# Kernel optimization log

Hardware: AMD Instinct MI355X
Metric: run time of the kernel (lower is better)

Reference implementation:

```python
import jax, jax.numpy as jnp
import numpy as np

D, K, HID, NBLK, N = 128, 256, 256, 2, 4096

def setup_inputs() -> dict:
    key = jax.random.key(0)
    ks = jax.random.split(key, 12)
    inp = {
        'x': jax.random.normal(ks[0], (N, D), jnp.float32),
        'x_hat': jax.random.normal(ks[1], (N, D), jnp.float32),
        'base_codebook': jax.random.normal(ks[2], (K, D), jnp.float32) * 0.1,
        # concat_proj: Linear(2D -> D), torch weight layout (out, in)
        'Wp': jax.random.normal(ks[3], (D, 2 * D), jnp.float32) / np.sqrt(2 * D),
        'bp': jnp.zeros((D,), jnp.float32),
        # residual blocks stacked over NBLK: Linear(D->HID), ReLU, Linear(HID->D)
        'W1': jax.random.normal(ks[4], (NBLK, HID, D), jnp.float32) / np.sqrt(D),
        'b1': jnp.zeros((NBLK, HID), jnp.float32),
        'W2': jax.random.normal(ks[5], (NBLK, D, HID), jnp.float32) / np.sqrt(HID),
        'b2': jnp.zeros((NBLK, D), jnp.float32),
    }
    return inp

def _forward(x, x_hat, base_codebook, Wp, bp, W1, b1, W2, b2):
    # concat_proj([x_hat, cbar]) decomposed: avoids materializing (N,K,2D)
    x_part = x_hat @ Wp[:, :D].T                      # (N, D)
    c_part = base_codebook @ Wp[:, D:].T + bp          # (K, D)
    C = x_part[:, None, :] + c_part[None, :, :]        # (N, K, D)
    for i in range(NBLK):
        h = jax.nn.relu(jnp.einsum('nkd,hd->nkh', C, W1[i]) + b1[i])
        C = C + jnp.einsum('nkh,dh->nkd', h, W2[i]) + b2[i]
    r = x - x_hat                                      # (N, D)
    dists = jnp.sum((r[:, None, :] - C) ** 2, axis=-1) # (N, K)
    codes = jnp.argmin(dists, axis=-1)                 # (N,)
    c_sel = jnp.take_along_axis(C, codes[:, None, None], axis=1)[:, 0, :]
    x_hat_new = x_hat + c_sel
    return codes, x_hat_new, r, c_sel

def reference(x, x_hat, base_codebook, Wp, bp, W1, b1, W2, b2):
    return _forward(x, x_hat, base_codebook, Wp, bp, W1, b1, W2, b2)
```

## Files before the change

### kernel.cpp

```cpp
#include <hip/hip_runtime.h>


#define QD    128
#define QK    256
#define QHID  256
#define QNBLK 2
#define QN    4096

typedef _Float16 f16;
typedef _Float16 f16x8  __attribute__((ext_vector_type(8)));
typedef float    f32x16 __attribute__((ext_vector_type(16)));
typedef unsigned u32x2  __attribute__((ext_vector_type(2)));

#define WS_CPART 0
#define WS_W1H   131072
#define WS_W1L   262144
#define WS_W2H   393216
#define WS_W2L   524288

#define L_WBUF  0
#define L_B1    98304
#define L_B2    100352
#define L_REDD  101376
#define L_REDI  102400
#define L_XP    103424
#define L_XH    103936
#define L_RS    104448
#define L_CSEL  104960
#define L_TOTAL 105472

static __device__ __forceinline__ f32x16 MF32(f16x8 a, f16x8 b, f32x16 c) {
    return __builtin_amdgcn_mfma_f32_32x32x16_f16(a, b, c, 0, 0, 0);
}
static __device__ __forceinline__ unsigned pkrtz(float a, float b) {
    return __builtin_bit_cast(unsigned, __builtin_amdgcn_cvt_pkrtz(a, b));
}
static __device__ __forceinline__ float f32lo(unsigned p) {
    return (float)__builtin_bit_cast(f16, (unsigned short)(p & 0xffffu));
}
static __device__ __forceinline__ float f32hi(unsigned p) {
    return (float)__builtin_bit_cast(f16, (unsigned short)(p >> 16));
}
static __device__ __forceinline__ u32x2 plswap(unsigned a, unsigned b) {
    return __builtin_amdgcn_permlane32_swap(a, b, false, false);
}
static __device__ __forceinline__ void gload_lds16(const void* g, void* l) {
    __builtin_amdgcn_global_load_lds(
        (const __attribute__((address_space(1))) unsigned*)g,
        (__attribute__((address_space(3))) unsigned*)l, 16, 0, 0);
}

template<int RB>
static __device__ __forceinline__ void split_frags(f32x16 a, f16x8& fh, f16x8& fl) {
    unsigned P0 = pkrtz(a[RB + 0], a[RB + 1]);
    unsigned P1 = pkrtz(a[RB + 2], a[RB + 3]);
    unsigned Q0 = pkrtz(a[RB + 4], a[RB + 5]);
    unsigned Q1 = pkrtz(a[RB + 6], a[RB + 7]);
    unsigned L0 = pkrtz(a[RB + 0] - f32lo(P0), a[RB + 1] - f32hi(P0));
    unsigned L1 = pkrtz(a[RB + 2] - f32lo(P1), a[RB + 3] - f32hi(P1));
    unsigned L2 = pkrtz(a[RB + 4] - f32lo(Q0), a[RB + 5] - f32hi(Q0));
    unsigned L3 = pkrtz(a[RB + 6] - f32lo(Q1), a[RB + 7] - f32hi(Q1));
    u32x2 s0 = plswap(P0, Q0);
    u32x2 s1 = plswap(P1, Q1);
    u32x2 t0 = plswap(L0, L2);
    u32x2 t1 = plswap(L1, L3);
    uint4 hw = make_uint4(s0.x, s1.x, s0.y, s1.y);
    uint4 lw = make_uint4(t0.x, t1.x, t0.y, t1.y);
    fh = __builtin_bit_cast(f16x8, hw);
    fl = __builtin_bit_cast(f16x8, lw);
}

__global__ __launch_bounds__(128) void qinco_prep(
    const float* __restrict__ cb, const float* __restrict__ Wp,
    const float* __restrict__ bp, const float* __restrict__ W1,
    const float* __restrict__ W2, char* __restrict__ ws) {
    const int blk = blockIdx.x;
    const int t = threadIdx.x;
    __shared__ float row[QD];

    if (blk < 256) {
        float* cpart = (float*)(ws + WS_CPART);
        row[t] = cb[blk * QD + t];
        __syncthreads();
        float acc = bp[t];
        const float* wr = Wp + (size_t)t * (2 * QD) + QD;
        #pragma unroll 8
        for (int e = 0; e < QD; ++e) acc = fmaf(row[e], wr[e], acc);
        cpart[blk * QD + t] = acc;
    } else if (blk < 384) {
        if (t < 64) {
            const int cid = blk - 256;
            const int b = cid >> 6, hc = (cid >> 3) & 7, kc = cid & 7;
            const int m = t & 31, g = t >> 5;
            f16* w1h = (f16*)(ws + WS_W1H);
            f16* w1l = (f16*)(ws + WS_W1L);
            #pragma unroll
            for (int j = 0; j < 8; ++j) {
                float wv = W1[((size_t)b * QHID + hc * 32 + m) * QD + kc * 16 + g * 8 + j];
                f16 hi = (f16)wv;
                size_t idx = ((size_t)cid * 64 + t) * 8 + j;
                w1h[idx] = hi;
                w1l[idx] = (f16)(wv - (float)hi);
            }
        }
    } else {
        if (t < 64) {
            const int e = blk - 384;
            const int b = e >> 6, hc = (e >> 3) & 7, dt = (e >> 1) & 3, kch = e & 1;
            const int m = t & 31, g = t >> 5;
            f16* w2h = (f16*)(ws + WS_W2H);
            f16* w2l = (f16*)(ws + WS_W2L);
            #pragma unroll
            for (int j = 0; j < 8; ++j) {
                float wv = W2[((size_t)b * QD + dt * 32 + m) * QHID + hc * 32 + kch * 16 + g * 8 + j];
                f16 hi = (f16)wv;
                size_t idx = ((size_t)e * 64 + t) * 8 + j;
                w2h[idx] = hi;
                w2l[idx] = (f16)(wv - (float)hi);
            }
        }
    }
}

__global__ __launch_bounds__(512, 2) void qinco_main(
    const float* __restrict__ x, const float* __restrict__ xh,
    const float* __restrict__ Wp,
    const float* __restrict__ b1g, const float* __restrict__ b2g,
    const char* __restrict__ ws, float* __restrict__ out) {

    extern __shared__ char smem[];
    const int n = blockIdx.x;
    const int t = threadIdx.x;
    const int w = t >> 6;
    const int l = t & 63;
    const int c32 = l & 31;
    const int g = l >> 5;
    const int baserow = w * 32;
    const int plane = w >> 1;
    const int jbase = (w & 1) * 4;

    float* b1_s  = (float*)(smem + L_B1);
    float* b2_s  = (float*)(smem + L_B2);
    float* red_d = (float*)(smem + L_REDD);
    int*   red_i = (int*)(smem + L_REDI);
    float* xp_s  = (float*)(smem + L_XP);
    float* xh_s  = (float*)(smem + L_XH);
    float* r_s   = (float*)(smem + L_RS);
    float* csel  = (float*)(smem + L_CSEL);

    const float* cpart = (const float*)(ws + WS_CPART);

    b1_s[t] = b1g[t];
    if (t < 2 * QD) b2_s[t] = b2g[t];
    if (t < QD) {
        float xv  = x[(size_t)n * QD + t];
        float xhv = xh[(size_t)n * QD + t];
        xh_s[t] = xhv;
        r_s[t]  = xv - xhv;
    }
    __syncthreads();

    if (t < QD) {
        const float4* wr = (const float4*)(Wp + (size_t)t * (2 * QD));
        const float4* xv = (const float4*)xh_s;
        float acc = 0.f;
        #pragma unroll
        for (int j = 0; j < QD / 4; ++j) {
            float4 a = wr[j], bv = xv[j];
            acc = fmaf(a.x, bv.x, acc);
            acc = fmaf(a.y, bv.y, acc);
            acc = fmaf(a.z, bv.z, acc);
            acc = fmaf(a.w, bv.w, acc);
        }
        xp_s[t] = acc;
    }
    __syncthreads();

    f32x16 Cacc[4];
    {
        const float* cprow = cpart + (size_t)(baserow + c32) * QD;
        #pragma unroll
        for (int dt = 0; dt < 4; ++dt)
            #pragma unroll
            for (int rq = 0; rq < 4; ++rq) {
                const int off = dt * 32 + 8 * rq + 4 * g;
                float4 cp  = *(const float4*)(cprow + off);
                float4 xp4 = *(const float4*)(xp_s + off);
                Cacc[dt][rq * 4 + 0] = cp.x + xp4.x;
                Cacc[dt][rq * 4 + 1] = cp.y + xp4.y;
                Cacc[dt][rq * 4 + 2] = cp.z + xp4.z;
                Cacc[dt][rq * 4 + 3] = cp.w + xp4.w;
            }
    }

    #pragma unroll
    for (int tt = 0; tt < 2; ++tt) {
        const char* s0 = ws + (size_t)(plane + 1) * 131072
                       + (size_t)(tt * 8 + jbase) * 1024 + (size_t)l * 16;
        char* d0 = smem + L_WBUF + (size_t)tt * 32768
                 + (size_t)(plane * 8 + jbase) * 1024;
        #pragma unroll
        for (int ii = 0; ii < 4; ++ii)
            gload_lds16(s0 + (size_t)ii * 1024, d0 + (size_t)ii * 1024);
    }

    f16x8 cfh[8], cfl[8];

    #pragma unroll 1
    for (int iter = 0; iter < 16; ++iter) {
        if (iter < 15) asm volatile("s_waitcnt vmcnt(4)" ::: "memory");
        else           asm volatile("s_waitcnt vmcnt(0)" ::: "memory");
        __builtin_amdgcn_s_barrier();
        asm volatile("" ::: "memory");

        if (iter < 14) {
            const int tt = iter + 2, bb = tt >> 3, hh = tt & 7;
            const char* s0 = ws + (size_t)(plane + 1) * 131072 + (size_t)bb * 65536
                           + (size_t)(hh * 8 + jbase) * 1024 + (size_t)l * 16;
            char* d0 = smem + L_WBUF + (size_t)(tt % 3) * 32768
                     + (size_t)(plane * 8 + jbase) * 1024;
            #pragma unroll
            for (int ii = 0; ii < 4; ++ii)
                gload_lds16(s0 + (size_t)ii * 1024, d0 + (size_t)ii * 1024);
        }

        const int b = iter >> 3;
        const int hc = iter & 7;

        if (hc == 0) {
            #pragma unroll
            for (int dt = 0; dt < 4; ++dt) {
                split_frags<0>(Cacc[dt], cfh[dt * 2 + 0], cfl[dt * 2 + 0]);
                split_frags<8>(Cacc[dt], cfh[dt * 2 + 1], cfl[dt * 2 + 1]);
            }
        }

        const char* wb = (const char*)smem + L_WBUF + (size_t)(iter % 3) * 32768
                       + (size_t)l * 16;

        f32x16 Ha;
        #pragma unroll
        for (int rq = 0; rq < 4; ++rq) {
            float4 bv = *(const float4*)(b1_s + b * QHID + hc * 32 + 8 * rq + 4 * g);
            Ha[rq * 4 + 0] = bv.x;
            Ha[rq * 4 + 1] = bv.y;
            Ha[rq * 4 + 2] = bv.z;
            Ha[rq * 4 + 3] = bv.w;
        }
        f16x8 wh = *(const f16x8*)(wb);
        f16x8 wl = *(const f16x8*)(wb + 8192);
        __builtin_amdgcn_s_setprio(1);
        #pragma unroll
        for (int kc = 0; kc < 8; ++kc) {
            f16x8 nh, nl;
            if (kc < 7) {
                nh = *(const f16x8*)(wb + (kc + 1) * 1024);
                nl = *(const f16x8*)(wb + 8192 + (kc + 1) * 1024);
            }
            Ha = MF32(wh, cfh[kc], Ha);
            Ha = MF32(wl, cfh[kc], Ha);
            Ha = MF32(wh, cfl[kc], Ha);
            if (kc < 7) { wh = nh; wl = nl; }
        }
        __builtin_amdgcn_s_setprio(0);

        #pragma unroll
        for (int r = 0; r < 16; ++r) Ha[r] = fmaxf(Ha[r], 0.f);

        f16x8 hfh0, hfl0, hfh1, hfl1;
        split_frags<0>(Ha, hfh0, hfl0);

        const char* q2h = wb + 16384;
        const char* q2l = wb + 24576;

        __builtin_amdgcn_s_setprio(1);
        #pragma unroll
        for (int dt = 0; dt < 4; ++dt) {
            f16x8 w2h0 = *(const f16x8*)(q2h + (size_t)(dt * 2) * 1024);
            f16x8 w2l0 = *(const f16x8*)(q2l + (size_t)(dt * 2) * 1024);
            Cacc[dt] = MF32(w2h0, hfh0, Cacc[dt]);
            Cacc[dt] = MF32(w2l0, hfh0, Cacc[dt]);
            Cacc[dt] = MF32(w2h0, hfl0, Cacc[dt]);
        }
        __builtin_amdgcn_s_setprio(0);

        split_frags<8>(Ha, hfh1, hfl1);

        __builtin_amdgcn_s_setprio(1);
        #pragma unroll
        for (int dt = 0; dt < 4; ++dt) {
            f16x8 w2h1 = *(const f16x8*)(q2h + (size_t)(dt * 2 + 1) * 1024);
            f16x8 w2l1 = *(const f16x8*)(q2l + (size_t)(dt * 2 + 1) * 1024);
            Cacc[dt] = MF32(w2h1, hfh1, Cacc[dt]);
            Cacc[dt] = MF32(w2l1, hfh1, Cacc[dt]);
            Cacc[dt] = MF32(w2h1, hfl1, Cacc[dt]);
        }
        __builtin_amdgcn_s_setprio(0);

        if (hc == 7) {
            #pragma unroll
            for (int dt = 0; dt < 4; ++dt)
                #pragma unroll
                for (int rq = 0; rq < 4; ++rq) {
                    float4 bv = *(const float4*)(b2_s + b * QD + dt * 32 + 8 * rq + 4 * g);
                    Cacc[dt][rq * 4 + 0] += bv.x;
                    Cacc[dt][rq * 4 + 1] += bv.y;
                    Cacc[dt][rq * 4 + 2] += bv.z;
                    Cacc[dt][rq * 4 + 3] += bv.w;
                }
        }
    }

    float pa = 0.f, pb = 0.f, pc = 0.f, pdm = 0.f;
    #pragma unroll
    for (int dt = 0; dt < 4; ++dt)
        #pragma unroll
        for (int rq = 0; rq < 4; ++rq) {
            float4 rr = *(const float4*)(r_s + dt * 32 + 8 * rq + 4 * g);
            float t0 = rr.x - Cacc[dt][rq * 4 + 0];
            float t1 = rr.y - Cacc[dt][rq * 4 + 1];
            float t2 = rr.z - Cacc[dt][rq * 4 + 2];
            float t3 = rr.w - Cacc[dt][rq * 4 + 3];
            pa = fmaf(t0, t0, pa);
            pb = fmaf(t1, t1, pb);
            pc = fmaf(t2, t2, pc);
            pdm = fmaf(t3, t3, pdm);
        }
    float pd = (pa + pb) + (pc + pdm);
    pd += __shfl_xor(pd, 32);
    if (l < 32) {
        red_d[baserow + l] = pd;
        red_i[baserow + l] = baserow + l;
    }
    __syncthreads();

    for (int off = 128; off > 0; off >>= 1) {
        if (t < off) {
            float d2 = red_d[t + off]; int i2 = red_i[t + off];
            float d1 = red_d[t];       int i1 = red_i[t];
            if (d2 < d1 || (d2 == d1 && i2 < i1)) { red_d[t] = d2; red_i[t] = i2; }
        }
        __syncthreads();
    }
    const int code = red_i[0];

    if (w == (code >> 5) && c32 == (code & 31)) {
        #pragma unroll
        for (int dt = 0; dt < 4; ++dt)
            #pragma unroll
            for (int rq = 0; rq < 4; ++rq)
                *(float4*)(csel + dt * 32 + 8 * rq + 4 * g) =
                    make_float4(Cacc[dt][rq * 4 + 0], Cacc[dt][rq * 4 + 1],
                                Cacc[dt][rq * 4 + 2], Cacc[dt][rq * 4 + 3]);
    }
    __syncthreads();

    if (t == 0) out[n] = (float)code;
    if (t < QD) {
        float cs  = csel[t];
        out[QN + (size_t)n * QD + t]                       = xh_s[t] + cs;
        out[QN + (size_t)QN * QD + (size_t)n * QD + t]     = r_s[t];
        out[QN + 2 * (size_t)QN * QD + (size_t)n * QD + t] = cs;
    }
}

extern "C" void kernel_launch(void* const* d_in, const int* in_sizes, int n_in,
                              void* d_out, int out_size, void* d_ws, size_t ws_size,
                              hipStream_t stream) {
    const float* x   = (const float*)d_in[0];
    const float* xh  = (const float*)d_in[1];
    const float* cb  = (const float*)d_in[2];
    const float* Wp  = (const float*)d_in[3];
    const float* bp  = (const float*)d_in[4];
    const float* W1  = (const float*)d_in[5];
    const float* b1  = (const float*)d_in[6];
    const float* W2  = (const float*)d_in[7];
    const float* b2  = (const float*)d_in[8];
    float* out = (float*)d_out;

    qinco_prep<<<512, 128, 0, stream>>>(cb, Wp, bp, W1, W2, (char*)d_ws);

    (void)hipFuncSetAttribute((const void*)qinco_main,
                              hipFuncAttributeMaxDynamicSharedMemorySize, L_TOTAL);
    qinco_main<<<QN, 512, L_TOTAL, stream>>>(x, xh, Wp, b1, b2,
                                             (const char*)d_ws, out);
}
```

Before: 717.1 us.

## Split each sample's codebook across two 256-thread blocks with a finalize kernel

Each sample's 256 candidate codes are now split across two blocks of 4 waves instead of one 8-wave block, with per-half argmin partials written to workspace. A new small kernel picks the winning half and writes the outputs, using the output buffer as scratch for the two candidate rows. The weight pipeline drops from triple-buffered prefetch two ahead to double-buffered prefetch one ahead with a full vmcnt(0) wait, which cuts LDS use so more blocks can fit per CU. In exchange, the work that does not depend on the code half (x_hat projection, bias loads, weight streaming) is done twice, and there is an extra launch and less prefetch depth.

Result: no change. 713.9 us (-0.4%).

```diff
diff --git a/kernel.cpp b/kernel.cpp
--- a/kernel.cpp
+++ b/kernel.cpp
@@ -17,17 +17,17 @@
 #define WS_W1L   262144
 #define WS_W2H   393216
 #define WS_W2L   524288
+#define WS_PART  655360
 
 #define L_WBUF  0
-#define L_B1    98304
-#define L_B2    100352
-#define L_REDD  101376
-#define L_REDI  102400
-#define L_XP    103424
-#define L_XH    103936
-#define L_RS    104448
-#define L_CSEL  104960
-#define L_TOTAL 105472
+#define L_B1    65536
+#define L_B2    67584
+#define L_REDD  68608
+#define L_REDI  69120
+#define L_XP    69632
+#define L_XH    70144
+#define L_RS    70656
+#define L_TOTAL 71168
 
 static __device__ __forceinline__ f32x16 MF32(f16x8 a, f16x8 b, f32x16 c) {
     return __builtin_amdgcn_mfma_f32_32x32x16_f16(a, b, c, 0, 0, 0);
@@ -122,22 +122,21 @@
     }
 }
 
-__global__ __launch_bounds__(512, 2) void qinco_main(
+__global__ __launch_bounds__(256, 2) void qinco_main(
     const float* __restrict__ x, const float* __restrict__ xh,
     const float* __restrict__ Wp,
     const float* __restrict__ b1g, const float* __restrict__ b2g,
-    const char* __restrict__ ws, float* __restrict__ out) {
+    char* __restrict__ ws, float* __restrict__ out) {
 
     extern __shared__ char smem[];
-    const int n = blockIdx.x;
+    const int n = blockIdx.x >> 1;
+    const int half = blockIdx.x & 1;
     const int t = threadIdx.x;
     const int w = t >> 6;
     const int l = t & 63;
     const int c32 = l & 31;
     const int g = l >> 5;
     const int baserow = w * 32;
-    const int plane = w >> 1;
-    const int jbase = (w & 1) * 4;
 
     float* b1_s  = (float*)(smem + L_B1);
     float* b2_s  = (float*)(smem + L_B2);
@@ -146,11 +145,11 @@
     float* xp_s  = (float*)(smem + L_XP);
     float* xh_s  = (float*)(smem + L_XH);
     float* r_s   = (float*)(smem + L_RS);
-    float* csel  = (float*)(smem + L_CSEL);
 
     const float* cpart = (const float*)(ws + WS_CPART);
 
     b1_s[t] = b1g[t];
+    b1_s[t + 256] = b1g[t + 256];
     if (t < 2 * QD) b2_s[t] = b2g[t];
     if (t < QD) {
         float xv  = x[(size_t)n * QD + t];
@@ -178,7 +177,7 @@
 
     f32x16 Cacc[4];
     {
-        const float* cprow = cpart + (size_t)(baserow + c32) * QD;
+        const float* cprow = cpart + (size_t)(half * 128 + baserow + c32) * QD;
         #pragma unroll
         for (int dt = 0; dt < 4; ++dt)
             #pragma unroll
@@ -193,14 +192,11 @@
             }
     }
 
-    #pragma unroll
-    for (int tt = 0; tt < 2; ++tt) {
-        const char* s0 = ws + (size_t)(plane + 1) * 131072
-                       + (size_t)(tt * 8 + jbase) * 1024 + (size_t)l * 16;
-        char* d0 = smem + L_WBUF + (size_t)tt * 32768
-                 + (size_t)(plane * 8 + jbase) * 1024;
-        #pragma unroll
-        for (int ii = 0; ii < 4; ++ii)
+    {
+        const char* s0 = ws + (size_t)(w + 1) * 131072 + (size_t)l * 16;
+        char* d0 = smem + L_WBUF + (size_t)w * 8192;
+        #pragma unroll
+        for (int ii = 0; ii < 8; ++ii)
             gload_lds16(s0 + (size_t)ii * 1024, d0 + (size_t)ii * 1024);
     }
 
@@ -208,19 +204,17 @@
 
     #pragma unroll 1
     for (int iter = 0; iter < 16; ++iter) {
-        if (iter < 15) asm volatile("s_waitcnt vmcnt(4)" ::: "memory");
-        else           asm volatile("s_waitcnt vmcnt(0)" ::: "memory");
+        asm volatile("s_waitcnt vmcnt(0)" ::: "memory");
         __builtin_amdgcn_s_barrier();
         asm volatile("" ::: "memory");
 
-        if (iter < 14) {
-            const int tt = iter + 2, bb = tt >> 3, hh = tt & 7;
-            const char* s0 = ws + (size_t)(plane + 1) * 131072 + (size_t)bb * 65536
-                           + (size_t)(hh * 8 + jbase) * 1024 + (size_t)l * 16;
-            char* d0 = smem + L_WBUF + (size_t)(tt % 3) * 32768
-                     + (size_t)(plane * 8 + jbase) * 1024;
-            #pragma unroll
-            for (int ii = 0; ii < 4; ++ii)
+        if (iter < 15) {
+            const int tt = iter + 1, bb = tt >> 3, hh = tt & 7;
+            const char* s0 = ws + (size_t)(w + 1) * 131072 + (size_t)bb * 65536
+                           + (size_t)hh * 8192 + (size_t)l * 16;
+            char* d0 = smem + L_WBUF + (size_t)(tt & 1) * 32768 + (size_t)w * 8192;
+            #pragma unroll
+            for (int ii = 0; ii < 8; ++ii)
                 gload_lds16(s0 + (size_t)ii * 1024, d0 + (size_t)ii * 1024);
         }
 
@@ -235,7 +229,7 @@
             }
         }
 
-        const char* wb = (const char*)smem + L_WBUF + (size_t)(iter % 3) * 32768
+        const char* wb = (const char*)smem + L_WBUF + (size_t)(iter & 1) * 32768
                        + (size_t)l * 16;
 
         f32x16 Ha;
@@ -334,7 +328,7 @@
     }
     __syncthreads();
 
-    for (int off = 128; off > 0; off >>= 1) {
+    for (int off = 64; off > 0; off >>= 1) {
         if (t < off) {
             float d2 = red_d[t + off]; int i2 = red_i[t + off];
             float d1 = red_d[t];       int i1 = red_i[t];
@@ -342,26 +336,50 @@
         }
         __syncthreads();
     }
-    const int code = red_i[0];
-
-    if (w == (code >> 5) && c32 == (code & 31)) {
+    const int lcode = red_i[0];
+
+    float* creg = out + (half == 0 ? (QN + 2 * (size_t)QN * QD) : (size_t)QN)
+                + (size_t)n * QD;
+    if (w == (lcode >> 5) && c32 == (lcode & 31)) {
         #pragma unroll
         for (int dt = 0; dt < 4; ++dt)
             #pragma unroll
             for (int rq = 0; rq < 4; ++rq)
-                *(float4*)(csel + dt * 32 + 8 * rq + 4 * g) =
+                *(float4*)(creg + dt * 32 + 8 * rq + 4 * g) =
                     make_float4(Cacc[dt][rq * 4 + 0], Cacc[dt][rq * 4 + 1],
                                 Cacc[dt][rq * 4 + 2], Cacc[dt][rq * 4 + 3]);
     }
-    __syncthreads();
-
-    if (t == 0) out[n] = (float)code;
-    if (t < QD) {
-        float cs  = csel[t];
-        out[QN + (size_t)n * QD + t]                       = xh_s[t] + cs;
-        out[QN + (size_t)QN * QD + (size_t)n * QD + t]     = r_s[t];
-        out[QN + 2 * (size_t)QN * QD + (size_t)n * QD + t] = cs;
-    }
+    if (t == 0) {
+        float2* pp = (float2*)(ws + WS_PART);
+        pp[n * 2 + half] = make_float2(red_d[0], (float)(half * 128 + lcode));
+    }
+}
+
+__global__ __launch_bounds__(128) void qinco_fin(
+    const float* __restrict__ x, const float* __restrict__ xh,
+    const char* __restrict__ ws, float* __restrict__ out) {
+    const int n = blockIdx.x;
+    const int t = threadIdx.x;
+    const float2* pp = (const float2*)(ws + WS_PART);
+    float2 p0 = pp[n * 2 + 0];
+    float2 p1 = pp[n * 2 + 1];
+    const int h = (p1.x < p0.x) ? 1 : 0;
+    const float codef = h ? p1.y : p0.y;
+
+    const size_t o_xh = QN + (size_t)n * QD;
+    const size_t o_r  = QN + (size_t)QN * QD + (size_t)n * QD;
+    const size_t o_cs = QN + 2 * (size_t)QN * QD + (size_t)n * QD;
+
+    float c0 = out[o_cs + t];
+    float c1 = out[o_xh + t];
+    float cs = h ? c1 : c0;
+    float xhv = xh[(size_t)n * QD + t];
+    float xv  = x[(size_t)n * QD + t];
+
+    if (t == 0) out[n] = codef;
+    out[o_xh + t] = xhv + cs;
+    out[o_r + t]  = xv - xhv;
+    out[o_cs + t] = cs;
 }
 
 extern "C" void kernel_launch(void* const* d_in, const int* in_sizes, int n_in,
@@ -382,6 +400,7 @@
 
     (void)hipFuncSetAttribute((const void*)qinco_main,
                               hipFuncAttributeMaxDynamicSharedMemorySize, L_TOTAL);
-    qinco_main<<<QN, 512, L_TOTAL, stream>>>(x, xh, Wp, b1, b2,
-                                             (const char*)d_ws, out);
-}
+    qinco_main<<<2 * QN, 256, L_TOTAL, stream>>>(x, xh, Wp, b1, b2,
+                                                 (char*)d_ws, out);
+    qinco_fin<<<QN, 128, 0, stream>>>(x, xh, (const char*)d_ws, out);
+}
```

## Stage whole W1 block in LDS and read W2 fragments directly from global

Applied to the files above, without the earlier changes.

Replaces the triple-buffered per-chunk LDS pipeline, which staged both W1 and W2 chunks with a barrier every iteration, with two restructurings. The full per-block W1 hi/lo planes (128 KB) are now loaded into LDS once per residual block. W2 fragments are loaded straight from global memory into registers at the start of each hidden chunk. This removes the 16 per-iteration barriers and the LDS traffic for W2, leaving only two synchronisation points per block. In exchange, LDS use grows to about 135 KB, which likely drops occupancy to one workgroup per CU. Global W2 load latency is also exposed, since each chunk's loads are issued just before use with no deeper prefetch.

After: 742.6 us. 1.04x slower.

```diff
diff --git a/kernel.cpp b/kernel.cpp
--- a/kernel.cpp
+++ b/kernel.cpp
@@ -14,20 +14,19 @@
 
 #define WS_CPART 0
 #define WS_W1H   131072
-#define WS_W1L   262144
 #define WS_W2H   393216
-#define WS_W2L   524288
-
-#define L_WBUF  0
-#define L_B1    98304
-#define L_B2    100352
-#define L_REDD  101376
-#define L_REDI  102400
-#define L_XP    103424
-#define L_XH    103936
-#define L_RS    104448
-#define L_CSEL  104960
-#define L_TOTAL 105472
+
+#define L_W1H   0
+#define L_W1L   65536
+#define L_B1    131072
+#define L_B2    133120
+#define L_REDD  134144
+#define L_REDI  135168
+#define L_XP    136192
+#define L_XH    136704
+#define L_RS    137216
+#define L_CSEL  137728
+#define L_TOTAL 138240
 
 static __device__ __forceinline__ f32x16 MF32(f16x8 a, f16x8 b, f32x16 c) {
     return __builtin_amdgcn_mfma_f32_32x32x16_f16(a, b, c, 0, 0, 0);
@@ -93,7 +92,7 @@
             const int b = cid >> 6, hc = (cid >> 3) & 7, kc = cid & 7;
             const int m = t & 31, g = t >> 5;
             f16* w1h = (f16*)(ws + WS_W1H);
-            f16* w1l = (f16*)(ws + WS_W1L);
+            f16* w1l = (f16*)(ws + WS_W1H + 131072);
             #pragma unroll
             for (int j = 0; j < 8; ++j) {
                 float wv = W1[((size_t)b * QHID + hc * 32 + m) * QD + kc * 16 + g * 8 + j];
@@ -109,7 +108,7 @@
             const int b = e >> 6, hc = (e >> 3) & 7, dt = (e >> 1) & 3, kch = e & 1;
             const int m = t & 31, g = t >> 5;
             f16* w2h = (f16*)(ws + WS_W2H);
-            f16* w2l = (f16*)(ws + WS_W2L);
+            f16* w2l = (f16*)(ws + WS_W2H + 131072);
             #pragma unroll
             for (int j = 0; j < 8; ++j) {
                 float wv = W2[((size_t)b * QD + dt * 32 + m) * QHID + hc * 32 + kch * 16 + g * 8 + j];
@@ -136,8 +135,6 @@
     const int c32 = l & 31;
     const int g = l >> 5;
     const int baserow = w * 32;
-    const int plane = w >> 1;
-    const int jbase = (w & 1) * 4;
 
     float* b1_s  = (float*)(smem + L_B1);
     float* b2_s  = (float*)(smem + L_B2);
@@ -150,6 +147,18 @@
 
     const float* cpart = (const float*)(ws + WS_CPART);
 
+    const size_t w1off = (size_t)w * 8192;
+    #define STAGE_W1(bb) {                                                     \
+        const char* s1h = ws + WS_W1H + (size_t)(bb) * 65536 + w1off            \
+                        + (size_t)l * 16;                                       \
+        const char* s1l = s1h + 131072;                                         \
+        char* d1h = smem + L_W1H + w1off;                                       \
+        char* d1l = smem + L_W1L + w1off;                                       \
+        _Pragma("unroll") for (int ii = 0; ii < 8; ++ii) {                      \
+            gload_lds16(s1h + (size_t)ii * 1024, d1h + (size_t)ii * 1024);      \
+            gload_lds16(s1l + (size_t)ii * 1024, d1l + (size_t)ii * 1024);      \
+        } }
+
     b1_s[t] = b1g[t];
     if (t < 2 * QD) b2_s[t] = b2g[t];
     if (t < QD) {
@@ -158,6 +167,7 @@
         xh_s[t] = xhv;
         r_s[t]  = xv - xhv;
     }
+    STAGE_W1(0)
     __syncthreads();
 
     if (t < QD) {
@@ -193,121 +203,101 @@
             }
     }
 
-    #pragma unroll
-    for (int tt = 0; tt < 2; ++tt) {
-        const char* s0 = ws + (size_t)(plane + 1) * 131072
-                       + (size_t)(tt * 8 + jbase) * 1024 + (size_t)l * 16;
-        char* d0 = smem + L_WBUF + (size_t)tt * 32768
-                 + (size_t)(plane * 8 + jbase) * 1024;
-        #pragma unroll
-        for (int ii = 0; ii < 4; ++ii)
-            gload_lds16(s0 + (size_t)ii * 1024, d0 + (size_t)ii * 1024);
-    }
-
     f16x8 cfh[8], cfl[8];
 
     #pragma unroll 1
-    for (int iter = 0; iter < 16; ++iter) {
-        if (iter < 15) asm volatile("s_waitcnt vmcnt(4)" ::: "memory");
-        else           asm volatile("s_waitcnt vmcnt(0)" ::: "memory");
-        __builtin_amdgcn_s_barrier();
-        asm volatile("" ::: "memory");
-
-        if (iter < 14) {
-            const int tt = iter + 2, bb = tt >> 3, hh = tt & 7;
-            const char* s0 = ws + (size_t)(plane + 1) * 131072 + (size_t)bb * 65536
-                           + (size_t)(hh * 8 + jbase) * 1024 + (size_t)l * 16;
-            char* d0 = smem + L_WBUF + (size_t)(tt % 3) * 32768
-                     + (size_t)(plane * 8 + jbase) * 1024;
-            #pragma unroll
-            for (int ii = 0; ii < 4; ++ii)
-                gload_lds16(s0 + (size_t)ii * 1024, d0 + (size_t)ii * 1024);
-        }
-
-        const int b = iter >> 3;
-        const int hc = iter & 7;
-
-        if (hc == 0) {
+    for (int b = 0; b < QNBLK; ++b) {
+        if (b == 1) {
+            __syncthreads();
+            STAGE_W1(1)
+            __syncthreads();
+        }
+
+        #pragma unroll
+        for (int dt = 0; dt < 4; ++dt) {
+            split_frags<0>(Cacc[dt], cfh[dt * 2 + 0], cfl[dt * 2 + 0]);
+            split_frags<8>(Cacc[dt], cfh[dt * 2 + 1], cfl[dt * 2 + 1]);
+        }
+
+        #pragma unroll 1
+        for (int hc = 0; hc < 8; ++hc) {
+            const char* pw2h = ws + WS_W2H + (size_t)b * 65536 + (size_t)hc * 8192
+                             + (size_t)l * 16;
+            const char* pw2l = pw2h + 131072;
+            f16x8 A0h[4], A0l[4], A1h[4], A1l[4];
             #pragma unroll
             for (int dt = 0; dt < 4; ++dt) {
-                split_frags<0>(Cacc[dt], cfh[dt * 2 + 0], cfl[dt * 2 + 0]);
-                split_frags<8>(Cacc[dt], cfh[dt * 2 + 1], cfl[dt * 2 + 1]);
-            }
-        }
-
-        const char* wb = (const char*)smem + L_WBUF + (size_t)(iter % 3) * 32768
-                       + (size_t)l * 16;
-
-        f32x16 Ha;
-        #pragma unroll
-        for (int rq = 0; rq < 4; ++rq) {
-            float4 bv = *(const float4*)(b1_s + b * QHID + hc * 32 + 8 * rq + 4 * g);
-            Ha[rq * 4 + 0] = bv.x;
-            Ha[rq * 4 + 1] = bv.y;
-            Ha[rq * 4 + 2] = bv.z;
-            Ha[rq * 4 + 3] = bv.w;
-        }
-        f16x8 wh = *(const f16x8*)(wb);
-        f16x8 wl = *(const f16x8*)(wb + 8192);
-        __builtin_amdgcn_s_setprio(1);
-        #pragma unroll
-        for (int kc = 0; kc < 8; ++kc) {
-            f16x8 nh, nl;
-            if (kc < 7) {
-                nh = *(const f16x8*)(wb + (kc + 1) * 1024);
-                nl = *(const f16x8*)(wb + 8192 + (kc + 1) * 1024);
-            }
-            Ha = MF32(wh, cfh[kc], Ha);
-            Ha = MF32(wl, cfh[kc], Ha);
-            Ha = MF32(wh, cfl[kc], Ha);
-            if (kc < 7) { wh = nh; wl = nl; }
-        }
-        __builtin_amdgcn_s_setprio(0);
-
-        #pragma unroll
-        for (int r = 0; r < 16; ++r) Ha[r] = fmaxf(Ha[r], 0.f);
-
-        f16x8 hfh0, hfl0, hfh1, hfl1;
-        split_frags<0>(Ha, hfh0, hfl0);
-
-        const char* q2h = wb + 16384;
-        const char* q2l = wb + 24576;
-
-        __builtin_amdgcn_s_setprio(1);
-        #pragma unroll
-        for (int dt = 0; dt < 4; ++dt) {
-            f16x8 w2h0 = *(const f16x8*)(q2h + (size_t)(dt * 2) * 1024);
-            f16x8 w2l0 = *(const f16x8*)(q2l + (size_t)(dt * 2) * 1024);
-            Cacc[dt] = MF32(w2h0, hfh0, Cacc[dt]);
-            Cacc[dt] = MF32(w2l0, hfh0, Cacc[dt]);
-            Cacc[dt] = MF32(w2h0, hfl0, Cacc[dt]);
-        }
-        __builtin_amdgcn_s_setprio(0);
-
-        split_frags<8>(Ha, hfh1, hfl1);
-
-        __builtin_amdgcn_s_setprio(1);
-        #pragma unroll
-        for (int dt = 0; dt < 4; ++dt) {
-            f16x8 w2h1 = *(const f16x8*)(q2h + (size_t)(dt * 2 + 1) * 1024);
-            f16x8 w2l1 = *(const f16x8*)(q2l + (size_t)(dt * 2 + 1) * 1024);
-            Cacc[dt] = MF32(w2h1, hfh1, Cacc[dt]);
-            Cacc[dt] = MF32(w2l1, hfh1, Cacc[dt]);
-            Cacc[dt] = MF32(w2h1, hfl1, Cacc[dt]);
-        }
-        __builtin_amdgcn_s_setprio(0);
-
-        if (hc == 7) {
-            #pragma unroll
-            for (int dt = 0; dt < 4; ++dt)
+                A0h[dt] = *(const f16x8*)(pw2h + dt * 2048);
+                A0l[dt] = *(const f16x8*)(pw2l + dt * 2048);
+                A1h[dt] = *(const f16x8*)(pw2h + dt * 2048 + 1024);
+                A1l[dt] = *(const f16x8*)(pw2l + dt * 2048 + 1024);
+            }
+
+            const char* wb1 = (const char*)smem + L_W1H + (size_t)hc * 8192
+                            + (size_t)l * 16;
+            f32x16 Ha;
+            #pragma unroll
+            for (int rq = 0; rq < 4; ++rq) {
+                float4 bv = *(const float4*)(b1_s + b * QHID + hc * 32 + 8 * rq + 4 * g);
+                Ha[rq * 4 + 0] = bv.x;
+                Ha[rq * 4 + 1] = bv.y;
+                Ha[rq * 4 + 2] = bv.z;
+                Ha[rq * 4 + 3] = bv.w;
+            }
+            f16x8 wh = *(const f16x8*)(wb1);
+            f16x8 wl = *(const f16x8*)(wb1 + 65536);
+            __builtin_amdgcn_s_setprio(1);
+            #pragma unroll
+            for (int kc = 0; kc < 8; ++kc) {
+                f16x8 nh, nl;
+                if (kc < 7) {
+                    nh = *(const f16x8*)(wb1 + (kc + 1) * 1024);
+                    nl = *(const f16x8*)(wb1 + 65536 + (kc + 1) * 1024);
+                }
+                Ha = MF32(wh, cfh[kc], Ha);
+                Ha = MF32(wl, cfh[kc], Ha);
+                Ha = MF32(wh, cfl[kc], Ha);
+                if (kc < 7) { wh = nh; wl = nl; }
+            }
+            __builtin_amdgcn_s_setprio(0);
+
+            #pragma unroll
+            for (int r = 0; r < 16; ++r) Ha[r] = fmaxf(Ha[r], 0.f);
+            f16x8 hfh0, hfl0, hfh1, hfl1;
+            split_frags<0>(Ha, hfh0, hfl0);
+
+            __builtin_amdgcn_s_setprio(1);
+            #pragma unroll
+            for (int dt = 0; dt < 4; ++dt) {
+                Cacc[dt] = MF32(A0h[dt], hfh0, Cacc[dt]);
+                Cacc[dt] = MF32(A0l[dt], hfh0, Cacc[dt]);
+                Cacc[dt] = MF32(A0h[dt], hfl0, Cacc[dt]);
+            }
+            __builtin_amdgcn_s_setprio(0);
+
+            split_frags<8>(Ha, hfh1, hfl1);
+
+            __builtin_amdgcn_s_setprio(1);
+            #pragma unroll
+            for (int dt = 0; dt < 4; ++dt) {
+                Cacc[dt] = MF32(A1h[dt], hfh1, Cacc[dt]);
+                Cacc[dt] = MF32(A1l[dt], hfh1, Cacc[dt]);
+                Cacc[dt] = MF32(A1h[dt], hfl1, Cacc[dt]);
+            }
+            __builtin_amdgcn_s_setprio(0);
+
+            if (hc == 7) {
                 #pragma unroll
-                for (int rq = 0; rq < 4; ++rq) {
-                    float4 bv = *(const float4*)(b2_s + b * QD + dt * 32 + 8 * rq + 4 * g);
-                    Cacc[dt][rq * 4 + 0] += bv.x;
-                    Cacc[dt][rq * 4 + 1] += bv.y;
-                    Cacc[dt][rq * 4 + 2] += bv.z;
-                    Cacc[dt][rq * 4 + 3] += bv.w;
-                }
+                for (int dt = 0; dt < 4; ++dt)
+                    #pragma unroll
+                    for (int rq = 0; rq < 4; ++rq) {
+                        float4 bv = *(const float4*)(b2_s + b * QD + dt * 32 + 8 * rq + 4 * g);
+                        Cacc[dt][rq * 4 + 0] += bv.x;
+                        Cacc[dt][rq * 4 + 1] += bv.y;
+                        Cacc[dt][rq * 4 + 2] += bv.z;
+                        Cacc[dt][rq * 4 + 3] += bv.w;
+                    }
+            }
         }
     }
 
@@ -362,6 +352,7 @@
         out[QN + (size_t)QN * QD + (size_t)n * QD + t]     = r_s[t];
         out[QN + 2 * (size_t)QN * QD + (size_t)n * QD + t] = cs;
     }
+    #undef STAGE_W1
 }
 
 extern "C" void kernel_launch(void* const* d_in, const int* in_sizes, int n_in,
```
